# Kernel tuning notes

Hardware: AMD Instinct MI355X
Metric: run time of the kernel (lower is better)

## Reference

```python
import jax, jax.numpy as jnp
import numpy as np
from jax import lax

DN = ('NCHW', 'OIHW', 'NCHW')

def _conv(x, w, b):
    y = lax.conv_general_dilated(x, w, (1, 1), 'SAME', dimension_numbers=DN)
    return y + b[None, :, None, None]

def setup_inputs() -> dict:
    key = jax.random.key(0)
    ks = jax.random.split(key, 11)
    B, C, H, W = 8, 16, 64, 64
    hid, K = 128, 8192
    s = 0.02
    return {
        'x': jax.random.normal(ks[0], (B, C, H, W), jnp.float32),
        # encoder: Conv2d(C->hid,3x3), GELU, Conv2d(hid->hid,3x3), GELU
        'ew1': jax.random.normal(ks[1], (hid, C, 3, 3), jnp.float32) * s,
        'eb1': jnp.zeros((hid,), jnp.float32),
        'ew2': jax.random.normal(ks[2], (hid, hid, 3, 3), jnp.float32) * s,
        'eb2': jnp.zeros((hid,), jnp.float32),
        # codebook: Embedding(K, hid), init normal std=0.02
        'embed': jax.random.normal(ks[3], (K, hid), jnp.float32) * s,
        # decoder: Conv2d(hid->hid,3x3), GELU, Conv2d(hid->C,1x1), sigmoid
        'dw1': jax.random.normal(ks[4], (hid, hid, 3, 3), jnp.float32) * s,
        'db1': jnp.zeros((hid,), jnp.float32),
        'dw2': jax.random.normal(ks[5], (C, hid, 1, 1), jnp.float32) * s,
        'db2': jnp.zeros((C,), jnp.float32),
    }

def reference(x, ew1, eb1, ew2, eb2, embed, dw1, db1, dw2, db2):
    # --- encoder ---
    h = jax.nn.gelu(_conv(x, ew1, eb1), approximate=False)
    h = jax.nn.gelu(_conv(h, ew2, eb2), approximate=False)  # [B, D, H, W]
    B, D, H, W = h.shape
    flat = jnp.transpose(h, (0, 2, 3, 1)).reshape(B * H * W, D)  # [N, D]
    # --- VQ: pairwise sq-dist + argmin (no_grad in original) ---
    flat_ng = lax.stop_gradient(flat)
    d2 = (jnp.sum(flat_ng * flat_ng, axis=1, keepdims=True)
          - 2.0 * flat_ng @ embed.T
          + jnp.sum(embed * embed, axis=1)[None, :])  # [N, K]
    idx = jnp.argmin(d2, axis=1)  # [N]
    z = idx.reshape(B, H, W)
    q = embed[idx].reshape(B, H, W, D)  # gather
    # --- decoder ---
    qc = jnp.transpose(q, (0, 3, 1, 2))  # NCHW
    y = jax.nn.gelu(_conv(qc, dw1, db1), approximate=False)
    x_hat = jax.nn.sigmoid(_conv(y, dw2, db2))  # [B, C, H, W]
    return x_hat
```

## Files before the change

### kernel.cpp

```cpp
#include <hip/hip_runtime.h>

constexpr int B_ = 8, H_ = 64, W_ = 64, C0 = 16, D_ = 128, K_ = 8192;
constexpr int N_ = B_ * H_ * W_;

typedef __attribute__((ext_vector_type(8))) short short8;
typedef __attribute__((ext_vector_type(4))) float f32x4;

__device__ __forceinline__ float gelu_f(float x) {
    return 0.5f * x * (1.0f + erff(x * 0.70710678118654752440f));
}

__device__ __forceinline__ unsigned short f2bf(float f) {
    unsigned u = __float_as_uint(f);
    u += 0x7fffu + ((u >> 16) & 1u);
    return (unsigned short)(u >> 16);
}

__device__ __forceinline__ void gload_lds16(const void* g, void* l) {
    __builtin_amdgcn_global_load_lds(
        (const __attribute__((address_space(1))) unsigned int*)g,
        (__attribute__((address_space(3))) unsigned int*)l, 16, 0, 0);
}

__global__ __launch_bounds__(256) void prep_kernel(
    const float* __restrict__ x, const float* __restrict__ ew1,
    const float* __restrict__ ew2, const float* __restrict__ dw1,
    const float* __restrict__ embed, unsigned short* __restrict__ xtbf,
    unsigned short* __restrict__ wtbf2, unsigned short* __restrict__ wtbf3,
    float* __restrict__ e2n, unsigned short* __restrict__ embbf,
    unsigned short* __restrict__ wtb1b,
    unsigned long long* __restrict__ partial,
    unsigned short* __restrict__ embq) {
    __shared__ float xt[16][66];
    int blk = blockIdx.x;
    int tid = threadIdx.x;
    if (blk < 512) {
        int b = blk >> 6, h = blk & 63;
        int c = tid >> 4, w4 = tid & 15;
        float4 v = ((const float4*)x)[(b * 16 + c) * 1024 + h * 16 + w4];
        xt[c][w4 * 4 + 0] = v.x;
        xt[c][w4 * 4 + 1] = v.y;
        xt[c][w4 * 4 + 2] = v.z;
        xt[c][w4 * 4 + 3] = v.w;
        __syncthreads();
        int w = tid >> 2, cg = (tid & 3) * 4;
        ushort4 o;
        o.x = f2bf(xt[cg + 0][w]);
        o.y = f2bf(xt[cg + 1][w]);
        o.z = f2bf(xt[cg + 2][w]);
        o.w = f2bf(xt[cg + 3][w]);
        *(ushort4*)(xtbf + (((b * 64 + h) * 64 + w) << 4) + cg) = o;
    } else if (blk < 1664) {
        const float* src = (blk < 1088) ? ew2 : dw1;
        unsigned short* dst = (blk < 1088) ? wtbf2 : wtbf3;
        int i = (blk - ((blk < 1088) ? 512 : 1088)) * 256 + tid;
        int g = i >> 12, rem = i & 4095;
        int ns = rem >> 9, q = (rem >> 7) & 3, r = (rem >> 3) & 15, e = rem & 7;
        int t = g >> 2, k = g & 3;
        int co = ns * 16 + r, ci = k * 32 + q * 8 + e;
        dst[i] = f2bf(src[(co * 128 + ci) * 9 + t]);
    } else if (blk < 1696) {
        int k = (blk - 1664) * 256 + tid;
        const float4* e4 = (const float4*)(embed + (size_t)k * 128);
        float s = 0.0f;
#pragma unroll 8
        for (int i = 0; i < 32; ++i) {
            float4 v = e4[i];
            s += v.x * v.x + v.y * v.y + v.z * v.z + v.w * v.w;
        }
        e2n[k] = -0.5f * s;
    } else if (blk < 2720) {
        int i = (blk - 1696) * 256 + tid;
        float4 v = ((const float4*)embed)[i];
        uint2 o;
        o.x = (unsigned)f2bf(v.x) | ((unsigned)f2bf(v.y) << 16);
        o.y = (unsigned)f2bf(v.z) | ((unsigned)f2bf(v.w) << 16);
        ((uint2*)embbf)[i] = o;
    } else if (blk < 2800) {
        int i = (blk - 2720) * 256 + tid;
        int co = i / 160, kk = i % 160;
        float v = 0.0f;
        if (kk < 144) {
            int t = kk >> 4, ci = kk & 15;
            v = ew1[(co * 16 + ci) * 9 + t];
        }
        wtb1b[i] = f2bf(v);
    } else if (blk < 2928) {
        int i = (blk - 2800) * 256 + tid;
        partial[i] = 0ULL;
    } else {
        int s = (blk - 2928) * 256 + tid;
        int T = s >> 10;
        int rem = s & 1023;
        int kk = rem >> 8, nsp = (rem >> 6) & 3, q = (rem >> 4) & 3,
            r = rem & 15;
        int code = T * 64 + nsp * 16 + r;
        int d0 = kk * 32 + q * 8;
        const float* ep = embed + (size_t)code * 128 + d0;
        unsigned short* op = embq + (size_t)s * 8;
#pragma unroll
        for (int e = 0; e < 8; ++e) op[e] = f2bf(ep[e]);
    }
}

__global__ __launch_bounds__(256, 2) void conv1_mfma_kernel(
    const unsigned short* __restrict__ xtbf,
    const unsigned short* __restrict__ wtb1b,
    const float* __restrict__ bias,
    unsigned short* __restrict__ out) {
    constexpr int LDA = 168;
    __shared__ __align__(16) unsigned short As[64 * LDA];
    int tid = threadIdx.x;
    int wv = tid >> 6, lane = tid & 63;
    int r = lane & 15, q = lane >> 4;
    int h0 = blockIdx.x & 63, b = blockIdx.x >> 6;

    short8 bf1[5][2];
#pragma unroll
    for (int k = 0; k < 5; ++k)
#pragma unroll
        for (int ns = 0; ns < 2; ++ns)
            bf1[k][ns] = *(const short8*)(wtb1b + (wv * 32 + ns * 16 + r) * 160 +
                                          k * 32 + q * 8);

#pragma unroll
    for (int j = 0; j < 5; ++j) {
        int s = tid + j * 256;
        if (s < 1152) {
            int px = s / 18, rem = s % 18;
            int t = rem >> 1, half = rem & 1;
            int hh = h0 + t / 3 - 1, ww = px + t % 3 - 1;
            float4 v = make_float4(0.f, 0.f, 0.f, 0.f);
            if ((unsigned)hh < 64u && (unsigned)ww < 64u)
                v = *(const float4*)(xtbf + (((b * 64 + hh) * 64 + ww) << 4) +
                                     half * 8);
            *(float4*)(As + px * LDA + t * 16 + half * 8) = v;
        } else {
            int z = s - 1152;
            int px = z >> 1, half = z & 1;
            *(float4*)(As + px * LDA + 144 + half * 8) =
                make_float4(0.f, 0.f, 0.f, 0.f);
        }
    }
    __syncthreads();

    f32x4 acc[4][2];
#pragma unroll
    for (int ms = 0; ms < 4; ++ms)
#pragma unroll
        for (int ns = 0; ns < 2; ++ns) acc[ms][ns] = (f32x4){0.f, 0.f, 0.f, 0.f};

#pragma unroll
    for (int k = 0; k < 5; ++k) {
        short8 af[4];
#pragma unroll
        for (int ms = 0; ms < 4; ++ms)
            af[ms] = *(const short8*)(As + (ms * 16 + r) * LDA + k * 32 + q * 8);
#pragma unroll
        for (int ms = 0; ms < 4; ++ms)
#pragma unroll
            for (int ns = 0; ns < 2; ++ns)
                acc[ms][ns] = __builtin_amdgcn_mfma_f32_16x16x32_bf16(
                    af[ms], bf1[k][ns], acc[ms][ns], 0, 0, 0);
    }

#pragma unroll
    for (int ns = 0; ns < 2; ++ns) {
        int co = wv * 32 + ns * 16 + r;
        float bv = bias[co];
#pragma unroll
        for (int ms = 0; ms < 4; ++ms)
#pragma unroll
            for (int rg = 0; rg < 4; ++rg) {
                int px = ms * 16 + q * 4 + rg;
                int pix = (b * 64 + h0) * 64 + px;
                out[(size_t)pix * 128 + co] = f2bf(gelu_f(acc[ms][ns][rg] + bv));
            }
    }
}

template <bool OUT_BF16, bool GATHER, bool FUSE>
__global__ __launch_bounds__(256, 2) void conv3x3_mfma_kernel(
    const unsigned short* __restrict__ in,
    const unsigned long long* __restrict__ gidx,
    const unsigned short* __restrict__ wtb,
    const float* __restrict__ bias,
    const float* __restrict__ w2,
    const float* __restrict__ b2,
    void* __restrict__ out_) {
    constexpr int LDC = 136;
    __shared__ __align__(16) unsigned short As[3 * 66 * LDC];
    __shared__ __align__(16) unsigned short Ws[2][4096];
    __shared__ __align__(16) float ws2[FUSE ? 2048 : 4];
    int tid = threadIdx.x;
    int wv = tid >> 6, lane = tid & 63;
    int r = lane & 15, q = lane >> 4;
    int h0 = blockIdx.x & 63, b = blockIdx.x >> 6;

    gload_lds16(wtb + (wv * 2) * 512 + lane * 8, &Ws[0][(wv * 2) * 512]);
    gload_lds16(wtb + (wv * 2 + 1) * 512 + lane * 8,
                &Ws[0][(wv * 2 + 1) * 512]);

    constexpr int NJ = FUSE ? 15 : 13;
    for (int j = 0; j < NJ; ++j) {
        int s = tid + j * 256;
        if (s < 3168) {
            int col = s >> 4, chunk = s & 15;
            int ry = col / 66, cx = col % 66;
            int hh = h0 - 1 + ry, ww = cx - 1;
            float4 v = make_float4(0.f, 0.f, 0.f, 0.f);
            if ((unsigned)hh < 64u && (unsigned)ww < 64u) {
                int pix = (b * 64 + hh) * 64 + ww;
                const unsigned short* src;
                if (GATHER) {
                    int k = 8191 - (int)(unsigned)(gidx[pix] & 0xFFFFFFFFu);
                    src = in + (size_t)k * 128;
                } else {
                    src = in + (size_t)pix * 128;
                }
                v = *(const float4*)(src + chunk * 8);
            }
            *(float4*)(As + col * LDC + chunk * 8) = v;
        } else if (FUSE && s < 3680) {
            int i = s - 3168;
            ((float4*)ws2)[i] = ((const float4*)w2)[i];
        }
    }
    __syncthreads();

    f32x4 acc[4][2];
#pragma unroll
    for (int ms = 0; ms < 4; ++ms)
#pragma unroll
        for (int ns = 0; ns < 2; ++ns) acc[ms][ns] = (f32x4){0.f, 0.f, 0.f, 0.f};

    int cur = 0;
#pragma unroll 4
    for (int g = 0; g < 36; ++g) {
        if (g < 35) {
            const unsigned short* wsrc = wtb + (size_t)(g + 1) * 4096;
            unsigned short* dst = &Ws[cur ^ 1][0];
            gload_lds16(wsrc + (wv * 2) * 512 + lane * 8, dst + (wv * 2) * 512);
            gload_lds16(wsrc + (wv * 2 + 1) * 512 + lane * 8,
                        dst + (wv * 2 + 1) * 512);
        }
        int t = g >> 2, k = g & 3;
        int dy = t / 3, dx = t - dy * 3;
        short8 bf0 = *(const short8*)(&Ws[cur][(wv * 2) * 512] + lane * 8);
        short8 bf1 = *(const short8*)(&Ws[cur][(wv * 2 + 1) * 512] + lane * 8);
        short8 af[4];
#pragma unroll
        for (int ms = 0; ms < 4; ++ms) {
            int col = dy * 66 + ms * 16 + r + dx;
            af[ms] = *(const short8*)(As + col * LDC + k * 32 + q * 8);
        }
#pragma unroll
        for (int ms = 0; ms < 4; ++ms) {
            acc[ms][0] = __builtin_amdgcn_mfma_f32_16x16x32_bf16(
                af[ms], bf0, acc[ms][0], 0, 0, 0);
            acc[ms][1] = __builtin_amdgcn_mfma_f32_16x16x32_bf16(
                af[ms], bf1, acc[ms][1], 0, 0, 0);
        }
        __syncthreads();
        cur ^= 1;
    }

    if (!FUSE) {
#pragma unroll
        for (int ns = 0; ns < 2; ++ns) {
            int co = wv * 32 + ns * 16 + r;
            float bv = bias[co];
#pragma unroll
            for (int ms = 0; ms < 4; ++ms)
#pragma unroll
                for (int rg = 0; rg < 4; ++rg) {
                    int px = ms * 16 + q * 4 + rg;
                    int pix = (b * 64 + h0) * 64 + px;
                    float g = gelu_f(acc[ms][ns][rg] + bv);
                    if (OUT_BF16)
                        ((unsigned short*)out_)[(size_t)pix * 128 + co] = f2bf(g);
                    else
                        ((float*)out_)[(size_t)pix * 128 + co] = g;
                }
        }
    } else {
        __syncthreads();
        float* gbuf = (float*)As;
#pragma unroll
        for (int ns = 0; ns < 2; ++ns) {
            int co = wv * 32 + ns * 16 + r;
            float bv = bias[co];
#pragma unroll
            for (int ms = 0; ms < 4; ++ms)
#pragma unroll
                for (int rg = 0; rg < 4; ++rg) {
                    int px = ms * 16 + q * 4 + rg;
                    gbuf[px * 132 + co] = gelu_f(acc[ms][ns][rg] + bv);
                }
        }
        __syncthreads();
        int w_ = tid & 63, c0 = (tid >> 6) * 4;
        float a4[4] = {b2[c0], b2[c0 + 1], b2[c0 + 2], b2[c0 + 3]};
#pragma unroll 4
        for (int ci = 0; ci < 128; ci += 4) {
            float4 yv = *(const float4*)&gbuf[w_ * 132 + ci];
#pragma unroll
            for (int jc = 0; jc < 4; ++jc) {
                float4 wv4 = *(const float4*)&ws2[(c0 + jc) * 128 + ci];
                a4[jc] += yv.x * wv4.x + yv.y * wv4.y + yv.z * wv4.z +
                          yv.w * wv4.w;
            }
        }
        float* outp = (float*)out_;
#pragma unroll
        for (int jc = 0; jc < 4; ++jc) {
            float v = 1.0f / (1.0f + expf(-a4[jc]));
            outp[(((size_t)b * 16 + c0 + jc) * 64 + h0) * 64 + w_] = v;
        }
    }
}

__global__ __launch_bounds__(256, 2) void vq_mfma_kernel(
    const unsigned short* __restrict__ flatbf,
    const unsigned short* __restrict__ embq,
    const float* __restrict__ e2n,
    unsigned long long* __restrict__ partial) {
    __shared__ __align__(16) unsigned short Bs[2][8192];
    int tid = threadIdx.x;
    int wv = tid >> 6, lane = tid & 63;
    int r = lane & 15, q = lane >> 4;
    int p_h = wv & 1;
    int c_s = wv >> 1;
    int half = blockIdx.x & 1;
    int m0 = (blockIdx.x >> 1) * 64;
    int kbase = half * 4096;
    int t0 = half * 64;

    short8 af[4][2];
#pragma unroll
    for (int kk = 0; kk < 4; ++kk)
#pragma unroll
        for (int ms = 0; ms < 2; ++ms)
            af[kk][ms] = *(const short8*)(
                flatbf + (size_t)(m0 + p_h * 32 + ms * 16 + r) * 128 +
                kk * 32 + q * 8);

    const float* e2p = e2n + kbase + c_s * 32 + r;
    float e2a = e2p[0], e2b = e2p[16];
    float e2nx0 = 0.f, e2nx1 = 0.f;

    {
        const unsigned short* src = embq + (size_t)t0 * 8192;
#pragma unroll
        for (int j = 0; j < 4; ++j) {
            int o = (j * 4 + wv) * 512;
            gload_lds16(src + o + lane * 8, &Bs[0][o]);
        }
    }

    float best[2][4];
#pragma unroll
    for (int ms = 0; ms < 2; ++ms)
#pragma unroll
        for (int rg = 0; rg < 4; ++rg) best[ms][rg] = -3.4e38f;

    __syncthreads();

    f32x4 acc[2][2];
#pragma unroll
    for (int ms = 0; ms < 2; ++ms) {
        acc[ms][0] = (f32x4){e2a, e2a, e2a, e2a};
        acc[ms][1] = (f32x4){e2b, e2b, e2b, e2b};
    }

    int cur = 0;
#pragma unroll 1
    for (int it = 0; it < 64; ++it) {
        if (it < 63) {
            const unsigned short* src = embq + (size_t)(t0 + it + 1) * 8192;
            unsigned short* dst = &Bs[cur ^ 1][0];
#pragma unroll
            for (int j = 0; j < 4; ++j) {
                int o = (j * 4 + wv) * 512;
                gload_lds16(src + o + lane * 8, dst + o);
            }
            e2nx0 = e2p[(it + 1) * 64];
            e2nx1 = e2p[(it + 1) * 64 + 16];
        }
        const unsigned short* bb = &Bs[cur][0];
#pragma unroll
        for (int kk = 0; kk < 4; ++kk) {
            short8 bf0 = *(const short8*)(bb + kk * 2048 + (c_s * 2) * 512 +
                                          q * 128 + r * 8);
            short8 bf1 = *(const short8*)(bb + kk * 2048 + (c_s * 2 + 1) * 512 +
                                          q * 128 + r * 8);
#pragma unroll
            for (int ms = 0; ms < 2; ++ms) {
                acc[ms][0] = __builtin_amdgcn_mfma_f32_16x16x32_bf16(
                    af[kk][ms], bf0, acc[ms][0], 0, 0, 0);
                acc[ms][1] = __builtin_amdgcn_mfma_f32_16x16x32_bf16(
                    af[kk][ms], bf1, acc[ms][1], 0, 0, 0);
            }
        }
        unsigned kb = (unsigned)(2047 - ((it & 31) * 64 + c_s * 32 + r));
#pragma unroll
        for (int ms = 0; ms < 2; ++ms)
#pragma unroll
            for (int rg = 0; rg < 4; ++rg) {
                float u0 = __uint_as_float(
                    (__float_as_uint(acc[ms][0][rg]) & 0xFFFFF800u) | kb);
                float u1 = __uint_as_float(
                    (__float_as_uint(acc[ms][1][rg]) & 0xFFFFF800u) |
                    (kb - 16u));
                best[ms][rg] = fmaxf(best[ms][rg], fmaxf(u0, u1));
            }
        if ((it & 31) == 31) {
#pragma unroll
            for (int ms = 0; ms < 2; ++ms)
#pragma unroll
                for (int rg = 0; rg < 4; ++rg) {
                    float v = best[ms][rg];
#pragma unroll
                    for (int m = 1; m < 16; m <<= 1)
                        v = fmaxf(v, __shfl_xor(v, m));
                    if (r == 0) {
                        unsigned bits = __float_as_uint(v);
                        int cand = 2047 - (int)(bits & 2047u);
                        int code = kbase + (it >> 5) * 2048 + cand;
                        unsigned sb = (bits & 0x80000000u) ? ~bits
                                                           : (bits | 0x80000000u);
                        unsigned long long packed =
                            ((unsigned long long)sb << 32) |
                            (unsigned)(8191 - code);
                        atomicMax(
                            partial + m0 + p_h * 32 + ms * 16 + q * 4 + rg,
                            packed);
                    }
                    best[ms][rg] = -3.4e38f;
                }
        }
        if (it < 63) {
#pragma unroll
            for (int ms = 0; ms < 2; ++ms) {
                acc[ms][0] = (f32x4){e2nx0, e2nx0, e2nx0, e2nx0};
                acc[ms][1] = (f32x4){e2nx1, e2nx1, e2nx1, e2nx1};
            }
        }
        __syncthreads();
        cur ^= 1;
    }
}

extern "C" void kernel_launch(void* const* d_in, const int* in_sizes, int n_in,
                              void* d_out, int out_size, void* d_ws,
                              size_t ws_size, hipStream_t stream) {
    const float* x = (const float*)d_in[0];
    const float* ew1 = (const float*)d_in[1];
    const float* eb1 = (const float*)d_in[2];
    const float* ew2 = (const float*)d_in[3];
    const float* eb2 = (const float*)d_in[4];
    const float* embed = (const float*)d_in[5];
    const float* dw1 = (const float*)d_in[6];
    const float* db1 = (const float*)d_in[7];
    const float* dw2 = (const float*)d_in[8];
    const float* db2 = (const float*)d_in[9];
    float* out = (float*)d_out;

    float* e2n = (float*)d_ws;
    unsigned long long* partial =
        (unsigned long long*)(e2n + 8192);
    unsigned short* xtbf = (unsigned short*)(partial + 32768);
    unsigned short* wtb1b = xtbf + 524288;
    unsigned short* wtbf2 = wtb1b + 20480;
    unsigned short* wtbf3 = wtbf2 + 147456;
    unsigned short* embbf = wtbf3 + 147456;
    unsigned short* abf = embbf + 1048576;
    unsigned short* flatbf = abf + 4194304;
    unsigned short* embq = flatbf + 4194304;

    prep_kernel<<<3440, 256, 0, stream>>>(x, ew1, ew2, dw1, embed, xtbf, wtbf2,
                                          wtbf3, e2n, embbf, wtb1b, partial,
                                          embq);
    conv1_mfma_kernel<<<512, 256, 0, stream>>>(xtbf, wtb1b, eb1, abf);
    conv3x3_mfma_kernel<true, false, false><<<512, 256, 0, stream>>>(
        abf, nullptr, wtbf2, eb2, nullptr, nullptr, flatbf);
    vq_mfma_kernel<<<1024, 256, 0, stream>>>(flatbf, embq, e2n, partial);
    conv3x3_mfma_kernel<false, true, true><<<512, 256, 0, stream>>>(
        embbf, partial, wtbf3, db1, dw2, db2, out);
}
```

Before: 211.0 us.

## Triple-buffer VQ codebook tiles with prefetch distance two and manual vmcnt waits

The VQ argmin kernel now keeps three LDS buffers for codebook tiles and prefetches two iterations ahead instead of one. The end-of-iteration __syncthreads is replaced by a partial s_waitcnt vmcnt plus a raw s_barrier at the top of each iteration. The e2n norms are loaded via inline-asm global loads into alternating register pairs. The goal is to hide global-to-LDS latency behind MFMA work, at the cost of more LDS per block (which may reduce occupancy) and fragile hand-counted vmcnt ordering.

```diff
diff --git a/kernel.cpp b/kernel.cpp
--- a/kernel.cpp
+++ b/kernel.cpp
@@ -21,6 +21,11 @@
         (const __attribute__((address_space(1))) unsigned int*)g,
         (__attribute__((address_space(3))) unsigned int*)l, 16, 0, 0);
 }
+
+#define GLOAD_F(dst, addr)                                     \
+    asm volatile("global_load_dword %0, %1, off"               \
+                 : "=v"(dst)                                   \
+                 : "v"(addr))
 
 __global__ __launch_bounds__(256) void prep_kernel(
     const float* __restrict__ x, const float* __restrict__ ew1,
@@ -325,7 +330,7 @@
     const unsigned short* __restrict__ embq,
     const float* __restrict__ e2n,
     unsigned long long* __restrict__ partial) {
-    __shared__ __align__(16) unsigned short Bs[2][8192];
+    __shared__ __align__(16) unsigned short Bs[3][8192];
     int tid = threadIdx.x;
     int wv = tid >> 6, lane = tid & 63;
     int r = lane & 15, q = lane >> 4;
@@ -346,16 +351,25 @@
                 kk * 32 + q * 8);
 
     const float* e2p = e2n + kbase + c_s * 32 + r;
-    float e2a = e2p[0], e2b = e2p[16];
-    float e2nx0 = 0.f, e2nx1 = 0.f;
+    float e2a0, e2a1, e2b0, e2b1;
 
     {
-        const unsigned short* src = embq + (size_t)t0 * 8192;
+        const unsigned short* s0 = embq + (size_t)t0 * 8192;
 #pragma unroll
         for (int j = 0; j < 4; ++j) {
             int o = (j * 4 + wv) * 512;
-            gload_lds16(src + o + lane * 8, &Bs[0][o]);
-        }
+            gload_lds16(s0 + o + lane * 8, &Bs[0][o]);
+        }
+        GLOAD_F(e2a0, e2p);
+        GLOAD_F(e2a1, e2p + 16);
+        const unsigned short* s1 = embq + (size_t)(t0 + 1) * 8192;
+#pragma unroll
+        for (int j = 0; j < 4; ++j) {
+            int o = (j * 4 + wv) * 512;
+            gload_lds16(s1 + o + lane * 8, &Bs[1][o]);
+        }
+        GLOAD_F(e2b0, e2p + 64);
+        GLOAD_F(e2b1, e2p + 80);
     }
 
     float best[2][4];
@@ -364,35 +378,57 @@
 #pragma unroll
         for (int rg = 0; rg < 4; ++rg) best[ms][rg] = -3.4e38f;
 
-    __syncthreads();
-
     f32x4 acc[2][2];
-#pragma unroll
-    for (int ms = 0; ms < 2; ++ms) {
-        acc[ms][0] = (f32x4){e2a, e2a, e2a, e2a};
-        acc[ms][1] = (f32x4){e2b, e2b, e2b, e2b};
-    }
-
-    int cur = 0;
-#pragma unroll 1
+    const unsigned short* pR = &Bs[0][0];
+    unsigned short* pW = &Bs[2][0];
+
+#pragma unroll 2
     for (int it = 0; it < 64; ++it) {
-        if (it < 63) {
-            const unsigned short* src = embq + (size_t)(t0 + it + 1) * 8192;
-            unsigned short* dst = &Bs[cur ^ 1][0];
+        if (it == 63) {
+            asm volatile("s_waitcnt vmcnt(0)" ::: "memory");
+        } else {
+            asm volatile("s_waitcnt vmcnt(6)" ::: "memory");
+        }
+        __builtin_amdgcn_sched_barrier(0);
+        __builtin_amdgcn_s_barrier();
+
+        {
+            float i0, i1;
+            if ((it & 1) == 0) {
+                i0 = e2a0;
+                i1 = e2a1;
+            } else {
+                i0 = e2b0;
+                i1 = e2b1;
+            }
+#pragma unroll
+            for (int ms = 0; ms < 2; ++ms) {
+                acc[ms][0] = (f32x4){i0, i0, i0, i0};
+                acc[ms][1] = (f32x4){i1, i1, i1, i1};
+            }
+        }
+
+        if (it < 62) {
+            const unsigned short* src = embq + (size_t)(t0 + it + 2) * 8192;
 #pragma unroll
             for (int j = 0; j < 4; ++j) {
                 int o = (j * 4 + wv) * 512;
-                gload_lds16(src + o + lane * 8, dst + o);
-            }
-            e2nx0 = e2p[(it + 1) * 64];
-            e2nx1 = e2p[(it + 1) * 64 + 16];
-        }
-        const unsigned short* bb = &Bs[cur][0];
+                gload_lds16(src + o + lane * 8, pW + o);
+            }
+            if ((it & 1) == 0) {
+                GLOAD_F(e2a0, e2p + (it + 2) * 64);
+                GLOAD_F(e2a1, e2p + (it + 2) * 64 + 16);
+            } else {
+                GLOAD_F(e2b0, e2p + (it + 2) * 64);
+                GLOAD_F(e2b1, e2p + (it + 2) * 64 + 16);
+            }
+        }
+
 #pragma unroll
         for (int kk = 0; kk < 4; ++kk) {
-            short8 bf0 = *(const short8*)(bb + kk * 2048 + (c_s * 2) * 512 +
+            short8 bf0 = *(const short8*)(pR + kk * 2048 + (c_s * 2) * 512 +
                                           q * 128 + r * 8);
-            short8 bf1 = *(const short8*)(bb + kk * 2048 + (c_s * 2 + 1) * 512 +
+            short8 bf1 = *(const short8*)(pR + kk * 2048 + (c_s * 2 + 1) * 512 +
                                           q * 128 + r * 8);
 #pragma unroll
             for (int ms = 0; ms < 2; ++ms) {
@@ -402,6 +438,7 @@
                     af[kk][ms], bf1, acc[ms][1], 0, 0, 0);
             }
         }
+
         unsigned kb = (unsigned)(2047 - ((it & 31) * 64 + c_s * 32 + r));
 #pragma unroll
         for (int ms = 0; ms < 2; ++ms)
@@ -439,15 +476,9 @@
                     best[ms][rg] = -3.4e38f;
                 }
         }
-        if (it < 63) {
-#pragma unroll
-            for (int ms = 0; ms < 2; ++ms) {
-                acc[ms][0] = (f32x4){e2nx0, e2nx0, e2nx0, e2nx0};
-                acc[ms][1] = (f32x4){e2nx1, e2nx1, e2nx1, e2nx1};
-            }
-        }
-        __syncthreads();
-        cur ^= 1;
+
+        pR = (pR == &Bs[2][0]) ? &Bs[0][0] : pR + 8192;
+        pW = (pW == &Bs[2][0]) ? &Bs[0][0] : pW + 8192;
     }
 }
 
```

Result: slower. 222.1 us (+5.3%).
